# Optimization experiments

Measured on AMD Instinct MI355X. Metric: run time of the kernel, lower is better.

The kernel has to match this reference:

```python
import jax, jax.numpy as jnp
import numpy as np

B, D, R = 8192, 4096, 64
REG_W, REG_C = 0.01, 0.05


def setup_inputs() -> dict:
    key = jax.random.key(0)
    ks = jax.random.split(key, 7)
    return {
        "X": jax.random.normal(ks[0], (B, D), dtype=jnp.float32),
        "U1": jax.random.normal(ks[1], (1, D, R), dtype=jnp.float32),
        "U2": jax.random.normal(ks[2], (2, D, R), dtype=jnp.float32),
        "U3": jax.random.normal(ks[3], (3, D, R), dtype=jnp.float32),
        "C": jax.random.normal(ks[4], (3,), dtype=jnp.float32),
        "beta": jax.random.normal(ks[5], (1,), dtype=jnp.float32),
        "C_sin": jax.random.normal(ks[6], (1,), dtype=jnp.float32),
    }


def reference(X, U1, U2, U3, C, beta, C_sin):
    # term_j(x) = sum_r prod_{i<=j} <x, U_j[i, :, r]>
    result = jnp.broadcast_to(beta[0], (X.shape[0],))
    reg_loss_w = jnp.float32(0.0)
    for j, U in enumerate((U1, U2, U3)):
        dots = jnp.einsum("bd,odr->obr", X, U)      # [order, B, R]
        term = jnp.prod(dots, axis=0).sum(axis=1)   # [B]
        result = result + C[j] * term
        reg_loss_w = reg_loss_w + REG_W * (jnp.abs(U).sum() / U.size)
    sine_term = C_sin[0] * jnp.sin(X).sum(axis=1)
    result = result + sine_term
    reg_loss_c = REG_C * (jnp.abs(C).sum() + jnp.abs(C_sin).sum())
    total_reg = reg_loss_w + reg_loss_c
    return result, total_reg
```

## Files before the change

### kernel.cpp

```cpp
#include <hip/hip_runtime.h>
#include <hip/hip_bf16.h>

typedef float f32x4 __attribute__((ext_vector_type(4)));
typedef short s16x8 __attribute__((ext_vector_type(8)));

#define D_DIM 4096
#define NT 24
#define BM 64
#define NBODY 16
#define AOFF 24576
#define SINW_OFF 3145728u
#define PART_OFF 3276800u

__device__ __forceinline__ unsigned short f2bf(float f) {
    unsigned u = __float_as_uint(f);
    u += 0x7fffu + ((u >> 16) & 1u);
    return (unsigned short)(u >> 16);
}

__device__ __forceinline__ void gload16(const void* g, void* l) {
    __builtin_amdgcn_global_load_lds(
        (const __attribute__((address_space(1))) unsigned int*)g,
        (__attribute__((address_space(3))) unsigned int*)l, 16, 0, 0);
}

__global__ __launch_bounds__(64) void reg_init_kernel(const float* __restrict__ C,
                                                      const float* __restrict__ Csin,
                                                      float* __restrict__ reg_out) {
    if (threadIdx.x == 0)
        reg_out[0] = 0.05f * (fabsf(C[0]) + fabsf(C[1]) + fabsf(C[2]) + fabsf(Csin[0]));
}

__global__ __launch_bounds__(64) void build_w_kernel(const float* __restrict__ U1,
                                                     const float* __restrict__ U2,
                                                     const float* __restrict__ U3,
                                                     unsigned short* __restrict__ W,
                                                     float* __restrict__ reg_out) {
    const int ks = blockIdx.x / NT;
    const int ct = blockIdx.x % NT;
    const int l  = threadIdx.x;
    const int n  = ct * 16 + (l & 15);
    const int kb = ks * 32 + ((l >> 4) << 3);

    const float* src;
    float scale;
    if (n < 64)       { src = U1 + n;                  scale = 0.01f / 262144.f; }
    else if (n < 128) { src = U2 + (n - 64);           scale = 0.01f / 524288.f; }
    else if (n < 192) { src = U2 + 262144 + (n - 128); scale = 0.01f / 524288.f; }
    else if (n < 256) { src = U3 + (n - 192);          scale = 0.01f / 786432.f; }
    else if (n < 320) { src = U3 + 262144 + (n - 256); scale = 0.01f / 786432.f; }
    else              { src = U3 + 524288 + (n - 320); scale = 0.01f / 786432.f; }

    unsigned short h[8];
    float sabs = 0.f;
#pragma unroll
    for (int j = 0; j < 8; ++j) {
        float u = src[(size_t)(kb + j) * 64];
        sabs += fabsf(u);
        h[j] = f2bf(u);
    }
    uint4 pk;
    pk.x = (unsigned)h[0] | ((unsigned)h[1] << 16);
    pk.y = (unsigned)h[2] | ((unsigned)h[3] << 16);
    pk.z = (unsigned)h[4] | ((unsigned)h[5] << 16);
    pk.w = (unsigned)h[6] | ((unsigned)h[7] << 16);
    *(uint4*)(W + ((size_t)blockIdx.x * 64 + l) * 8) = pk;

    sabs *= scale;
#pragma unroll
    for (int off = 32; off >= 1; off >>= 1)
        sabs += __shfl_xor(sabs, off, 64);
    if (l == 0) atomicAdd(reg_out, sabs);
}

__global__ __launch_bounds__(256, 3) void poly_main_kernel(const float* __restrict__ X,
                                                           const unsigned short* __restrict__ W,
                                                           _Float16* __restrict__ part,
                                                           float* __restrict__ sinws) {
    __shared__ __align__(16) char pool[32768];

    const int t    = threadIdx.x;
    const int lane = t & 63;
    const int wv   = t >> 6;
    const int bid  = blockIdx.x;
    const int rb   = bid >> 3;
    const int cs   = (bid >> 2) & 1;
    const int ks   = bid & 3;
    const int row0 = rb * BM;
    const bool doSin = (cs == 0);

    const int sr = t >> 2;
    const int q  = t & 3;
    const float* xp = X + (size_t)(row0 + sr) * D_DIM + ks * 1024 + q * 8;
    const int aw0 = AOFF + (sr >> 4) * 1024 + (((q << 4) | (sr & 15)) << 4);
    const int aw1 = aw0 + 4096;

    f32x4 acc[4][3];
#pragma unroll
    for (int r = 0; r < 4; ++r)
#pragma unroll
        for (int c = 0; c < 3; ++c) acc[r][c] = (f32x4){0.f, 0.f, 0.f, 0.f};
    float sinacc = 0.f;

    for (int d = 0; d < NBODY; ++d) {
        const size_t slabg = (size_t)(ks * 32 + 2 * d);
#pragma unroll
        for (int ksl = 0; ksl < 2; ++ksl)
#pragma unroll
            for (int j = 0; j < 3; ++j) {
                const unsigned short* g = W
                    + ((slabg + ksl) * 24 + cs * 12 + wv * 3 + j) * 512 + lane * 8;
                gload16(g, pool + ksl * 12288 + (wv * 3 + j) * 1024);
            }
#pragma unroll
        for (int ksl = 0; ksl < 2; ++ksl) {
            f32x4 a = *(const f32x4*)(xp + d * 64 + ksl * 32);
            f32x4 b = *(const f32x4*)(xp + d * 64 + ksl * 32 + 4);
            if (doSin)
                sinacc += __sinf(a.x) + __sinf(a.y) + __sinf(a.z) + __sinf(a.w)
                        + __sinf(b.x) + __sinf(b.y) + __sinf(b.z) + __sinf(b.w);
            uint4 pk;
            pk.x = (unsigned)f2bf(a.x) | ((unsigned)f2bf(a.y) << 16);
            pk.y = (unsigned)f2bf(a.z) | ((unsigned)f2bf(a.w) << 16);
            pk.z = (unsigned)f2bf(b.x) | ((unsigned)f2bf(b.y) << 16);
            pk.w = (unsigned)f2bf(b.z) | ((unsigned)f2bf(b.w) << 16);
            *(uint4*)(pool + (ksl ? aw1 : aw0)) = pk;
        }
        __syncthreads();

#pragma unroll
        for (int ksl = 0; ksl < 2; ++ksl) {
            s16x8 b0 = *(const s16x8*)(pool + ksl * 12288 + (wv * 3 + 0) * 1024 + lane * 16);
            s16x8 b1 = *(const s16x8*)(pool + ksl * 12288 + (wv * 3 + 1) * 1024 + lane * 16);
            s16x8 b2 = *(const s16x8*)(pool + ksl * 12288 + (wv * 3 + 2) * 1024 + lane * 16);
#pragma unroll
            for (int rf = 0; rf < 4; ++rf) {
                s16x8 af = *(const s16x8*)(pool + AOFF + (ksl * 4 + rf) * 1024 + lane * 16);
                acc[rf][0] = __builtin_amdgcn_mfma_f32_16x16x32_bf16(af, b0, acc[rf][0], 0, 0, 0);
                acc[rf][1] = __builtin_amdgcn_mfma_f32_16x16x32_bf16(af, b1, acc[rf][1], 0, 0, 0);
                acc[rf][2] = __builtin_amdgcn_mfma_f32_16x16x32_bf16(af, b2, acc[rf][2], 0, 0, 0);
            }
        }
        __syncthreads();
    }

    _Float16* pb = part + (size_t)ks * 8192 * 384;
    const int lr4 = (lane >> 4) << 2;
    const int lc  = lane & 15;
#pragma unroll
    for (int rf = 0; rf < 4; ++rf)
#pragma unroll
        for (int c = 0; c < 3; ++c) {
            const int col = cs * 192 + (wv * 3 + c) * 16 + lc;
#pragma unroll
            for (int i = 0; i < 4; ++i)
                pb[(size_t)(row0 + rf * 16 + lr4 + i) * 384 + col] = (_Float16)acc[rf][c][i];
        }

    if (doSin) {
        sinacc += __shfl_xor(sinacc, 1);
        sinacc += __shfl_xor(sinacc, 2);
        if (q == 0)
            sinws[(size_t)ks * 8192 + row0 + sr] = sinacc;
    }
}

__global__ __launch_bounds__(512) void combine_kernel(const _Float16* __restrict__ part,
                                                      const float* __restrict__ sinws,
                                                      const float* __restrict__ C,
                                                      const float* __restrict__ beta,
                                                      const float* __restrict__ Csin,
                                                      float* __restrict__ out) {
    const int t   = threadIdx.x;
    const int row = blockIdx.x * 32 + (t >> 4);
    const int cc  = t & 15;
    const size_t rbase = (size_t)row * 384;

    float t1 = 0.f, t2 = 0.f, t3 = 0.f;
#pragma unroll
    for (int j = 0; j < 4; ++j) {
        const int c = j * 16 + cc;
        float a1 = 0.f, a2 = 0.f, b2 = 0.f, a3 = 0.f, b3 = 0.f, c3 = 0.f;
#pragma unroll
        for (int qq = 0; qq < 4; ++qq) {
            const _Float16* p = part + (size_t)qq * 8192 * 384 + rbase;
            a1 += (float)p[c];
            a2 += (float)p[64 + c];
            b2 += (float)p[128 + c];
            a3 += (float)p[192 + c];
            b3 += (float)p[256 + c];
            c3 += (float)p[320 + c];
        }
        t1 += a1;
        t2 += a2 * b2;
        t3 += a3 * b3 * c3;
    }
#pragma unroll
    for (int off = 1; off < 16; off <<= 1) {
        t1 += __shfl_xor(t1, off, 16);
        t2 += __shfl_xor(t2, off, 16);
        t3 += __shfl_xor(t3, off, 16);
    }
    if (cc == 0) {
        const float s = sinws[row] + sinws[8192 + row]
                      + sinws[2 * 8192 + row] + sinws[3 * 8192 + row];
        out[row] = beta[0] + C[0] * t1 + C[1] * t2 + C[2] * t3 + Csin[0] * s;
    }
}

extern "C" void kernel_launch(void* const* d_in, const int* in_sizes, int n_in,
                              void* d_out, int out_size, void* d_ws, size_t ws_size,
                              hipStream_t stream) {
    const float* X   = (const float*)d_in[0];
    const float* U1  = (const float*)d_in[1];
    const float* U2  = (const float*)d_in[2];
    const float* U3  = (const float*)d_in[3];
    const float* Cc  = (const float*)d_in[4];
    const float* bet = (const float*)d_in[5];
    const float* Cs  = (const float*)d_in[6];
    float* out = (float*)d_out;

    unsigned short* W = (unsigned short*)d_ws;
    float* sinws = (float*)((char*)d_ws + SINW_OFF);
    _Float16* part = (_Float16*)((char*)d_ws + PART_OFF);

    reg_init_kernel<<<1, 64, 0, stream>>>(Cc, Cs, out + 8192);
    build_w_kernel<<<128 * NT, 64, 0, stream>>>(U1, U2, U3, W, out + 8192);
    poly_main_kernel<<<1024, 256, 0, stream>>>(X, W, part, sinws);
    combine_kernel<<<256, 512, 0, stream>>>(part, sinws, Cc, bet, Cs, out);
}
```

Before: 105.1 us.

## Retile main GEMM to 128x128 blocks with 2x2 wave grid

Changes the poly_main block tile from 64 rows by 192 columns to 128 rows by 128 columns. Four waves now form a 2x2 grid, each holding 4x4 MFMA fragments, and the K step per iteration is halved to 32. This aims to give each wave more fragment reuse per LDS read and use less shared memory. In exchange, X (fp32) is re-read across three column blocks instead of two, and the number of barrier-separated iterations doubles.

```diff
diff --git a/kernel.cpp b/kernel.cpp
--- a/kernel.cpp
+++ b/kernel.cpp
@@ -6,9 +6,9 @@
 
 #define D_DIM 4096
 #define NT 24
-#define BM 64
-#define NBODY 16
-#define AOFF 24576
+#define BM 128
+#define NBODY 32
+#define AOFF 8192
 #define SINW_OFF 3145728u
 #define PART_OFF 3276800u
 
@@ -77,91 +77,100 @@
                                                            const unsigned short* __restrict__ W,
                                                            _Float16* __restrict__ part,
                                                            float* __restrict__ sinws) {
-    __shared__ __align__(16) char pool[32768];
+    __shared__ __align__(16) char pool[16384];
 
     const int t    = threadIdx.x;
     const int lane = t & 63;
     const int wv   = t >> 6;
+    const int rg   = wv >> 1;
+    const int cgp  = wv & 1;
     const int bid  = blockIdx.x;
-    const int rb   = bid >> 3;
-    const int cs   = (bid >> 2) & 1;
-    const int ks   = bid & 3;
+    const int rb   = bid / 12;
+    const int cb   = (bid / 4) % 3;
+    const int kq   = bid & 3;
     const int row0 = rb * BM;
-    const bool doSin = (cs == 0);
-
-    const int sr = t >> 2;
-    const int q  = t & 3;
-    const float* xp = X + (size_t)(row0 + sr) * D_DIM + ks * 1024 + q * 8;
-    const int aw0 = AOFF + (sr >> 4) * 1024 + (((q << 4) | (sr & 15)) << 4);
-    const int aw1 = aw0 + 4096;
-
-    f32x4 acc[4][3];
+    const bool doSin = (cb == 0);
+
+    const int sr = t >> 1;
+    const int h  = t & 1;
+    const float* xp = X + (size_t)(row0 + sr) * D_DIM + kq * 1024 + h * 16;
+    const int rf_s = sr >> 4;
+    const int aw0 = AOFF + rf_s * 1024 + (((h * 2) * 16 + (sr & 15)) * 16);
+    const int aw1 = aw0 + 256;
+
+    f32x4 acc[4][4];
 #pragma unroll
     for (int r = 0; r < 4; ++r)
 #pragma unroll
-        for (int c = 0; c < 3; ++c) acc[r][c] = (f32x4){0.f, 0.f, 0.f, 0.f};
+        for (int c = 0; c < 4; ++c) acc[r][c] = (f32x4){0.f, 0.f, 0.f, 0.f};
     float sinacc = 0.f;
 
     for (int d = 0; d < NBODY; ++d) {
-        const size_t slabg = (size_t)(ks * 32 + 2 * d);
-#pragma unroll
-        for (int ksl = 0; ksl < 2; ++ksl)
-#pragma unroll
-            for (int j = 0; j < 3; ++j) {
-                const unsigned short* g = W
-                    + ((slabg + ksl) * 24 + cs * 12 + wv * 3 + j) * 512 + lane * 8;
-                gload16(g, pool + ksl * 12288 + (wv * 3 + j) * 1024);
-            }
-#pragma unroll
-        for (int ksl = 0; ksl < 2; ++ksl) {
-            f32x4 a = *(const f32x4*)(xp + d * 64 + ksl * 32);
-            f32x4 b = *(const f32x4*)(xp + d * 64 + ksl * 32 + 4);
+        {
+            const unsigned short* g = W
+                + ((size_t)(kq * 32 + d) * 24 + cb * 8 + 2 * wv) * 512 + lane * 8;
+            gload16(g, pool + (2 * wv) * 1024);
+            gload16(g + 512, pool + (2 * wv + 1) * 1024);
+        }
+        {
+            const float* xb = xp + d * 32;
+            f32x4 a = *(const f32x4*)xb;
+            f32x4 b = *(const f32x4*)(xb + 4);
+            f32x4 c = *(const f32x4*)(xb + 8);
+            f32x4 e = *(const f32x4*)(xb + 12);
             if (doSin)
                 sinacc += __sinf(a.x) + __sinf(a.y) + __sinf(a.z) + __sinf(a.w)
-                        + __sinf(b.x) + __sinf(b.y) + __sinf(b.z) + __sinf(b.w);
-            uint4 pk;
-            pk.x = (unsigned)f2bf(a.x) | ((unsigned)f2bf(a.y) << 16);
-            pk.y = (unsigned)f2bf(a.z) | ((unsigned)f2bf(a.w) << 16);
-            pk.z = (unsigned)f2bf(b.x) | ((unsigned)f2bf(b.y) << 16);
-            pk.w = (unsigned)f2bf(b.z) | ((unsigned)f2bf(b.w) << 16);
-            *(uint4*)(pool + (ksl ? aw1 : aw0)) = pk;
+                        + __sinf(b.x) + __sinf(b.y) + __sinf(b.z) + __sinf(b.w)
+                        + __sinf(c.x) + __sinf(c.y) + __sinf(c.z) + __sinf(c.w)
+                        + __sinf(e.x) + __sinf(e.y) + __sinf(e.z) + __sinf(e.w);
+            uint4 lo, hi;
+            lo.x = (unsigned)f2bf(a.x) | ((unsigned)f2bf(a.y) << 16);
+            lo.y = (unsigned)f2bf(a.z) | ((unsigned)f2bf(a.w) << 16);
+            lo.z = (unsigned)f2bf(b.x) | ((unsigned)f2bf(b.y) << 16);
+            lo.w = (unsigned)f2bf(b.z) | ((unsigned)f2bf(b.w) << 16);
+            hi.x = (unsigned)f2bf(c.x) | ((unsigned)f2bf(c.y) << 16);
+            hi.y = (unsigned)f2bf(c.z) | ((unsigned)f2bf(c.w) << 16);
+            hi.z = (unsigned)f2bf(e.x) | ((unsigned)f2bf(e.y) << 16);
+            hi.w = (unsigned)f2bf(e.z) | ((unsigned)f2bf(e.w) << 16);
+            *(uint4*)(pool + aw0) = lo;
+            *(uint4*)(pool + aw1) = hi;
         }
         __syncthreads();
 
-#pragma unroll
-        for (int ksl = 0; ksl < 2; ++ksl) {
-            s16x8 b0 = *(const s16x8*)(pool + ksl * 12288 + (wv * 3 + 0) * 1024 + lane * 16);
-            s16x8 b1 = *(const s16x8*)(pool + ksl * 12288 + (wv * 3 + 1) * 1024 + lane * 16);
-            s16x8 b2 = *(const s16x8*)(pool + ksl * 12288 + (wv * 3 + 2) * 1024 + lane * 16);
-#pragma unroll
-            for (int rf = 0; rf < 4; ++rf) {
-                s16x8 af = *(const s16x8*)(pool + AOFF + (ksl * 4 + rf) * 1024 + lane * 16);
-                acc[rf][0] = __builtin_amdgcn_mfma_f32_16x16x32_bf16(af, b0, acc[rf][0], 0, 0, 0);
-                acc[rf][1] = __builtin_amdgcn_mfma_f32_16x16x32_bf16(af, b1, acc[rf][1], 0, 0, 0);
-                acc[rf][2] = __builtin_amdgcn_mfma_f32_16x16x32_bf16(af, b2, acc[rf][2], 0, 0, 0);
-            }
+        s16x8 bf0 = *(const s16x8*)(pool + (cgp * 4 + 0) * 1024 + lane * 16);
+        s16x8 bf1 = *(const s16x8*)(pool + (cgp * 4 + 1) * 1024 + lane * 16);
+        s16x8 bf2 = *(const s16x8*)(pool + (cgp * 4 + 2) * 1024 + lane * 16);
+        s16x8 bf3 = *(const s16x8*)(pool + (cgp * 4 + 3) * 1024 + lane * 16);
+#pragma unroll
+        for (int r = 0; r < 4; ++r) {
+            s16x8 af = *(const s16x8*)(pool + AOFF + (rg * 4 + r) * 1024 + lane * 16);
+            acc[r][0] = __builtin_amdgcn_mfma_f32_16x16x32_bf16(af, bf0, acc[r][0], 0, 0, 0);
+            acc[r][1] = __builtin_amdgcn_mfma_f32_16x16x32_bf16(af, bf1, acc[r][1], 0, 0, 0);
+            acc[r][2] = __builtin_amdgcn_mfma_f32_16x16x32_bf16(af, bf2, acc[r][2], 0, 0, 0);
+            acc[r][3] = __builtin_amdgcn_mfma_f32_16x16x32_bf16(af, bf3, acc[r][3], 0, 0, 0);
         }
         __syncthreads();
     }
 
-    _Float16* pb = part + (size_t)ks * 8192 * 384;
+    _Float16* pb = part + (size_t)kq * 8192 * 384;
     const int lr4 = (lane >> 4) << 2;
     const int lc  = lane & 15;
 #pragma unroll
-    for (int rf = 0; rf < 4; ++rf)
-#pragma unroll
-        for (int c = 0; c < 3; ++c) {
-            const int col = cs * 192 + (wv * 3 + c) * 16 + lc;
-#pragma unroll
-            for (int i = 0; i < 4; ++i)
-                pb[(size_t)(row0 + rf * 16 + lr4 + i) * 384 + col] = (_Float16)acc[rf][c][i];
+    for (int r = 0; r < 4; ++r)
+#pragma unroll
+        for (int c = 0; c < 4; ++c) {
+            const int col = cb * 128 + cgp * 64 + c * 16 + lc;
+#pragma unroll
+            for (int i = 0; i < 4; ++i) {
+                const int rl = rg * 64 + r * 16 + lr4 + i;
+                pb[(size_t)(row0 + rl) * 384 + col] = (_Float16)acc[r][c][i];
+            }
         }
 
     if (doSin) {
         sinacc += __shfl_xor(sinacc, 1);
-        sinacc += __shfl_xor(sinacc, 2);
-        if (q == 0)
-            sinws[(size_t)ks * 8192 + row0 + sr] = sinacc;
+        if (h == 0)
+            sinws[(size_t)kq * 8192 + row0 + sr] = sinacc;
     }
 }
 
@@ -226,6 +235,6 @@
 
     reg_init_kernel<<<1, 64, 0, stream>>>(Cc, Cs, out + 8192);
     build_w_kernel<<<128 * NT, 64, 0, stream>>>(U1, U2, U3, W, out + 8192);
-    poly_main_kernel<<<1024, 256, 0, stream>>>(X, W, part, sinws);
+    poly_main_kernel<<<768, 256, 0, stream>>>(X, W, part, sinws);
     combine_kernel<<<256, 512, 0, stream>>>(part, sinws, Cc, bet, Cs, out);
 }
```

After: 111.4 us. 1.06x slower.
